# Performance work log

Measured on AMD Instinct MI355X. Metric: run time of the kernel, lower is better.

## Reference

```python
import jax, jax.numpy as jnp
import numpy as np

N, H, W, CIN, C = 2048, 19, 19, 256, 32
EPS = 1e-3

def setup_inputs() -> dict:
    key = jax.random.key(0)
    ks = jax.random.split(key, 14)
    return {
        "x": jax.random.normal(ks[0], (N, H, W, CIN), jnp.float32),
        "w_p": jax.random.normal(ks[1], (CIN, C), jnp.float32) * 0.05,
        "w_g": jax.random.normal(ks[2], (CIN, C), jnp.float32) * 0.05,
        "beta_g": jax.random.normal(ks[3], (C,), jnp.float32) * 0.1,
        "mean_g": jax.random.normal(ks[4], (C,), jnp.float32) * 0.1,
        "var_g": jax.random.uniform(ks[5], (C,), jnp.float32, 0.5, 1.5),
        "w_bias": jax.random.normal(ks[6], (2 * C, C), jnp.float32) * 0.1,
        "b_bias": jax.random.normal(ks[7], (C,), jnp.float32) * 0.1,
        "beta_p": jax.random.normal(ks[8], (C,), jnp.float32) * 0.1,
        "mean_p": jax.random.normal(ks[9], (C,), jnp.float32) * 0.1,
        "var_p": jax.random.uniform(ks[10], (C,), jnp.float32, 0.5, 1.5),
        "w_out": jax.random.normal(ks[11], (C, 2), jnp.float32) * 0.1,
        "w_pass": jax.random.normal(ks[12], (2 * C, 2), jnp.float32) * 0.1,
        "b_pass": jax.random.normal(ks[13], (2,), jnp.float32) * 0.1,
    }

def reference(x, w_p, w_g, beta_g, mean_g, var_g, w_bias, b_bias,
              beta_p, mean_p, var_p, w_out, w_pass, b_pass):
    # 1x1 convs (no bias) == channel matmuls
    p = jnp.einsum('nhwc,cd->nhwd', x, w_p)            # [N,H,W,C]
    g = jnp.einsum('nhwc,cd->nhwd', x, w_g)            # [N,H,W,C]
    # BN (scale=False, inference stats) + relu on g
    g = (g - mean_g) / jnp.sqrt(var_g + EPS) + beta_g
    g = jax.nn.relu(g)
    # global pool: per-channel mean & max over spatial dims -> [N, 2C]
    g_pooled = jnp.concatenate([g.mean(axis=(1, 2)), g.max(axis=(1, 2))], axis=1)
    # channelwise broadcast bias from pooled features
    bias = g_pooled @ w_bias + b_bias                  # [N,C]
    p = p + bias[:, None, None, :]
    # BN (scale=False) + relu on p
    p = (p - mean_p) / jnp.sqrt(var_p + EPS) + beta_p
    p = jax.nn.relu(p)
    # move logits: 1x1 conv to 2 channels
    pi = jnp.einsum('nhwc,ck->nhwk', p, w_out)         # [N,H,W,2]
    pass_logits = g_pooled @ w_pass + b_pass - 3.0     # [N,2]
    n = x.shape[0]
    pi_main = jnp.concatenate([pi[..., 0].reshape(n, -1), pass_logits[:, 0:1]], axis=1)
    pi_aux = jnp.concatenate([pi[..., 1].reshape(n, -1), pass_logits[:, 1:2]], axis=1)
    return pi_main, pi_aux
```

## Files before the change

kernel.cpp:

```cpp
#include <hip/hip_runtime.h>


#define N_IMG 2048
#define HW    361
#define CIN   256
#define C     32
#define NPIX  (N_IMG * HW)
#define EPSV  1e-3f

#define MT 256
#define KT 32
#define NT 64

#define WS_P_OFF    0
#define WS_PSUM_OFF ((size_t)NPIX * 32)
#define WS_PMAX_OFF (WS_PSUM_OFF + (size_t)N_IMG * C)
#define WS_BIAS_OFF (WS_PMAX_OFF + (size_t)N_IMG * C)

__global__ __launch_bounds__(256, 2) void k1_gemm_pool(
    const float* __restrict__ x,
    const float* __restrict__ w_p, const float* __restrict__ w_g,
    const float* __restrict__ beta_g, const float* __restrict__ mean_g,
    const float* __restrict__ var_g, float* __restrict__ ws)
{
    __shared__ float xs[KT][MT];
    __shared__ float wsh[KT][NT];

    const int t  = threadIdx.x;
    const int tm = t >> 3;
    const int tn = t & 7;
    const long P0 = (long)blockIdx.x * MT;

    float acc[8][8];
#pragma unroll
    for (int i = 0; i < 8; ++i)
#pragma unroll
        for (int j = 0; j < 8; ++j) acc[i][j] = 0.f;

    const float* xrow = x + (P0 + t) * (long)CIN;
    const int wr = t >> 3, wpart = t & 7;

    for (int k0 = 0; k0 < CIN; k0 += KT) {
#pragma unroll
        for (int i = 0; i < KT / 4; ++i) {
            float4 v = *(const float4*)(xrow + k0 + i * 4);
            xs[i * 4 + 0][t] = v.x;
            xs[i * 4 + 1][t] = v.y;
            xs[i * 4 + 2][t] = v.z;
            xs[i * 4 + 3][t] = v.w;
        }
        {
            const float* src = (wpart < 4) ? (w_p + (long)(k0 + wr) * C + wpart * 8)
                                           : (w_g + (long)(k0 + wr) * C + (wpart - 4) * 8);
            float4 v0 = *(const float4*)(src);
            float4 v1 = *(const float4*)(src + 4);
            *(float4*)(&wsh[wr][wpart * 8])     = v0;
            *(float4*)(&wsh[wr][wpart * 8 + 4]) = v1;
        }
        __syncthreads();
#pragma unroll
        for (int kk = 0; kk < KT; ++kk) {
            float a[8], b[8];
            *(float4*)(a)     = *(const float4*)(&xs[kk][tm * 8]);
            *(float4*)(a + 4) = *(const float4*)(&xs[kk][tm * 8 + 4]);
            *(float4*)(b)     = *(const float4*)(&wsh[kk][tn * 8]);
            *(float4*)(b + 4) = *(const float4*)(&wsh[kk][tn * 8 + 4]);
#pragma unroll
            for (int i = 0; i < 8; ++i)
#pragma unroll
                for (int j = 0; j < 8; ++j)
                    acc[i][j] = fmaf(a[i], b[j], acc[i][j]);
        }
        __syncthreads();
    }

    if (tn < 4) {
        float* wp_out = ws + WS_P_OFF;
#pragma unroll
        for (int i = 0; i < 8; ++i) {
            long pix = P0 + tm * 8 + i;
            float4 v0 = make_float4(acc[i][0], acc[i][1], acc[i][2], acc[i][3]);
            float4 v1 = make_float4(acc[i][4], acc[i][5], acc[i][6], acc[i][7]);
            *(float4*)(wp_out + pix * 32 + tn * 8)     = v0;
            *(float4*)(wp_out + pix * 32 + tn * 8 + 4) = v1;
        }
    }

    float gsum[2][8], gmax[2][8];
#pragma unroll
    for (int s = 0; s < 2; ++s)
#pragma unroll
        for (int j = 0; j < 8; ++j) { gsum[s][j] = 0.f; gmax[s][j] = 0.f; }

    const int  n0 = (int)(P0 / HW);
    const long Bnd = (long)(n0 + 1) * HW;

    if (tn >= 4) {
#pragma unroll
        for (int j = 0; j < 8; ++j) {
            int c = (tn - 4) * 8 + j;
            float rs = rsqrtf(var_g[c] + EPSV);
            float mg = mean_g[c], bg = beta_g[c];
#pragma unroll
            for (int i = 0; i < 8; ++i) {
                long pix = P0 + tm * 8 + i;
                float g = fmaxf((acc[i][j] - mg) * rs + bg, 0.f);
                int s = (pix >= Bnd) ? 1 : 0;
                gsum[s][j] += g;
                gmax[s][j] = fmaxf(gmax[s][j], g);
            }
        }
    }

#pragma unroll
    for (int s = 0; s < 2; ++s)
#pragma unroll
        for (int j = 0; j < 8; ++j) {
            float v = gsum[s][j], m = gmax[s][j];
            v += __shfl_xor(v, 8, 64);  m = fmaxf(m, __shfl_xor(m, 8, 64));
            v += __shfl_xor(v, 16, 64); m = fmaxf(m, __shfl_xor(m, 16, 64));
            v += __shfl_xor(v, 32, 64); m = fmaxf(m, __shfl_xor(m, 32, 64));
            gsum[s][j] = v; gmax[s][j] = m;
        }

    const int lane = t & 63;
    if (tn >= 4 && (lane >> 3) == 0) {
        float* psum = ws + WS_PSUM_OFF;
        int*   pmax = (int*)(ws + WS_PMAX_OFF);
#pragma unroll
        for (int s = 0; s < 2; ++s) {
            int n = n0 + s;
            bool active = (s == 0) || (Bnd < P0 + MT && n < N_IMG);
            if (active) {
#pragma unroll
                for (int j = 0; j < 8; ++j) {
                    int c = (tn - 4) * 8 + j;
                    atomicAdd(psum + n * C + c, gsum[s][j]);
                    atomicMax(pmax + n * C + c, __float_as_int(gmax[s][j]));
                }
            }
        }
    }
}

__global__ void k2_bias(const float* __restrict__ psum,
                        const float* __restrict__ pmax,
                        const float* __restrict__ w_bias,
                        const float* __restrict__ b_bias,
                        const float* __restrict__ w_pass,
                        const float* __restrict__ b_pass,
                        float* __restrict__ ws_bias,
                        float* __restrict__ out)
{
    const int n = blockIdx.x;
    const int t = threadIdx.x;
    __shared__ float gp[64];
    if (t < 32) gp[t] = psum[n * 32 + t] * (1.f / (float)HW);
    else        gp[t] = pmax[n * 32 + (t - 32)];
    __syncthreads();
    if (t < 32) {
        float acc = b_bias[t];
#pragma unroll
        for (int j = 0; j < 64; ++j) acc = fmaf(gp[j], w_bias[j * 32 + t], acc);
        ws_bias[n * 32 + t] = acc;
    } else if (t < 34) {
        int k = t - 32;
        float acc = b_pass[k] - 3.0f;
#pragma unroll
        for (int j = 0; j < 64; ++j) acc = fmaf(gp[j], w_pass[j * 2 + k], acc);
        out[(size_t)k * ((size_t)N_IMG * 362) + (size_t)n * 362 + 361] = acc;
    }
}

__global__ __launch_bounds__(256) void k3_epilogue(
    const float* __restrict__ ws_p, const float* __restrict__ ws_bias,
    const float* __restrict__ beta_p, const float* __restrict__ mean_p,
    const float* __restrict__ var_p, const float* __restrict__ w_out,
    float* __restrict__ out)
{
    const long pix = (long)blockIdx.x * 256 + threadIdx.x;
    const int n  = (int)(pix / HW);
    const int hw = (int)(pix - (long)n * HW);

    float p[32], b[32];
    const float4* pr = (const float4*)(ws_p + pix * 32);
    const float4* br = (const float4*)(ws_bias + (long)n * 32);
#pragma unroll
    for (int i = 0; i < 8; ++i) ((float4*)p)[i] = pr[i];
#pragma unroll
    for (int i = 0; i < 8; ++i) ((float4*)b)[i] = br[i];

    float a0 = 0.f, a1 = 0.f;
#pragma unroll
    for (int c = 0; c < 32; ++c) {
        float v = (p[c] + b[c] - mean_p[c]) * rsqrtf(var_p[c] + EPSV) + beta_p[c];
        v = fmaxf(v, 0.f);
        a0 = fmaf(v, w_out[c * 2 + 0], a0);
        a1 = fmaf(v, w_out[c * 2 + 1], a1);
    }
    out[(size_t)n * 362 + hw] = a0;
    out[(size_t)N_IMG * 362 + (size_t)n * 362 + hw] = a1;
}

extern "C" void kernel_launch(void* const* d_in, const int* in_sizes, int n_in,
                              void* d_out, int out_size, void* d_ws, size_t ws_size,
                              hipStream_t stream)
{
    const float* x      = (const float*)d_in[0];
    const float* w_p    = (const float*)d_in[1];
    const float* w_g    = (const float*)d_in[2];
    const float* beta_g = (const float*)d_in[3];
    const float* mean_g = (const float*)d_in[4];
    const float* var_g  = (const float*)d_in[5];
    const float* w_bias = (const float*)d_in[6];
    const float* b_bias = (const float*)d_in[7];
    const float* beta_p = (const float*)d_in[8];
    const float* mean_p = (const float*)d_in[9];
    const float* var_p  = (const float*)d_in[10];
    const float* w_out  = (const float*)d_in[11];
    const float* w_pass = (const float*)d_in[12];
    const float* b_pass = (const float*)d_in[13];
    float* out = (float*)d_out;
    float* ws  = (float*)d_ws;
    (void)in_sizes; (void)n_in; (void)out_size; (void)ws_size;

    hipMemsetAsync(ws + WS_PSUM_OFF, 0, 2u * N_IMG * C * sizeof(float), stream);

    k1_gemm_pool<<<NPIX / MT, 256, 0, stream>>>(x, w_p, w_g, beta_g, mean_g, var_g, ws);
    k2_bias<<<N_IMG, 64, 0, stream>>>(ws + WS_PSUM_OFF, ws + WS_PMAX_OFF,
                                      w_bias, b_bias, w_pass, b_pass,
                                      ws + WS_BIAS_OFF, out);
    k3_epilogue<<<NPIX / 256, 256, 0, stream>>>(ws + WS_P_OFF, ws + WS_BIAS_OFF,
                                                beta_p, mean_p, var_p, w_out, out);
}
```

Measured before the change: 1.116 ms.

## Use split-bf16 MFMA for the 1x1 conv GEMM and fuse bias into epilogue

Replaces the FP32 FMA GEMM with bf16 MFMA instructions, using a hi/lo split of both operands (three MFMAs per tile) to approximate FP32 accuracy. Weights are pre-split and transposed into workspace by a new prep kernel and staged whole in shared memory. The separate bias and epilogue kernels are merged into one per-image kernel that folds the BN and bias into a per-channel scale and offset. The split-bf16 scheme gives slightly lower accuracy than full FP32, and x is now read straight from global memory into registers without shared-memory staging.

```diff
diff --git a/kernel.cpp b/kernel.cpp
--- a/kernel.cpp
+++ b/kernel.cpp
@@ -1,4 +1,5 @@
 #include <hip/hip_runtime.h>
+#include <hip/hip_bf16.h>
 
 
 #define N_IMG 2048
@@ -7,199 +8,225 @@
 #define C     32
 #define NPIX  (N_IMG * HW)
 #define EPSV  1e-3f
-
-#define MT 256
-#define KT 32
-#define NT 64
+#define OUT_HALF (N_IMG * 362)
+
+#define KPAD  264
 
 #define WS_P_OFF    0
 #define WS_PSUM_OFF ((size_t)NPIX * 32)
 #define WS_PMAX_OFF (WS_PSUM_OFF + (size_t)N_IMG * C)
-#define WS_BIAS_OFF (WS_PMAX_OFF + (size_t)N_IMG * C)
+#define WS_WT_OFF   (WS_PMAX_OFF + (size_t)N_IMG * C)
+
+typedef __attribute__((ext_vector_type(8))) short short8;
+typedef __attribute__((ext_vector_type(4))) float f32x4;
+
+static __device__ __forceinline__ short f2bf(float f) {
+    __hip_bfloat16 h = __float2bfloat16(f);
+    return *reinterpret_cast<short*>(&h);
+}
+static __device__ __forceinline__ float bf2f(short s) {
+    unsigned int u = ((unsigned int)(unsigned short)s) << 16;
+    return __builtin_bit_cast(float, u);
+}
+
+__global__ void k0_prep(const float* __restrict__ w_p, const float* __restrict__ w_g,
+                        unsigned short* __restrict__ wt)
+{
+    const int col = blockIdx.x;
+    const int t = threadIdx.x;
+#pragma unroll
+    for (int it = 0; it < 2; ++it) {
+        int kk = t + it * 256;
+        if (kk < KPAD) {
+            unsigned short hi = 0, lo = 0;
+            if (kk < CIN) {
+                float f = (col < C) ? w_p[kk * C + col] : w_g[kk * C + (col - C)];
+                short h = f2bf(f);
+                hi = (unsigned short)h;
+                lo = (unsigned short)f2bf(f - bf2f(h));
+            }
+            wt[col * KPAD + kk] = hi;
+            wt[64 * KPAD + col * KPAD + kk] = lo;
+        }
+    }
+}
 
 __global__ __launch_bounds__(256, 2) void k1_gemm_pool(
     const float* __restrict__ x,
-    const float* __restrict__ w_p, const float* __restrict__ w_g,
+    const unsigned short* __restrict__ wt_g,
     const float* __restrict__ beta_g, const float* __restrict__ mean_g,
-    const float* __restrict__ var_g, float* __restrict__ ws)
-{
-    __shared__ float xs[KT][MT];
-    __shared__ float wsh[KT][NT];
-
-    const int t  = threadIdx.x;
-    const int tm = t >> 3;
-    const int tn = t & 7;
-    const long P0 = (long)blockIdx.x * MT;
-
-    float acc[8][8];
-#pragma unroll
-    for (int i = 0; i < 8; ++i)
-#pragma unroll
-        for (int j = 0; j < 8; ++j) acc[i][j] = 0.f;
-
-    const float* xrow = x + (P0 + t) * (long)CIN;
-    const int wr = t >> 3, wpart = t & 7;
-
-    for (int k0 = 0; k0 < CIN; k0 += KT) {
-#pragma unroll
-        for (int i = 0; i < KT / 4; ++i) {
-            float4 v = *(const float4*)(xrow + k0 + i * 4);
-            xs[i * 4 + 0][t] = v.x;
-            xs[i * 4 + 1][t] = v.y;
-            xs[i * 4 + 2][t] = v.z;
-            xs[i * 4 + 3][t] = v.w;
-        }
-        {
-            const float* src = (wpart < 4) ? (w_p + (long)(k0 + wr) * C + wpart * 8)
-                                           : (w_g + (long)(k0 + wr) * C + (wpart - 4) * 8);
-            float4 v0 = *(const float4*)(src);
-            float4 v1 = *(const float4*)(src + 4);
-            *(float4*)(&wsh[wr][wpart * 8])     = v0;
-            *(float4*)(&wsh[wr][wpart * 8 + 4]) = v1;
-        }
-        __syncthreads();
-#pragma unroll
-        for (int kk = 0; kk < KT; ++kk) {
-            float a[8], b[8];
-            *(float4*)(a)     = *(const float4*)(&xs[kk][tm * 8]);
-            *(float4*)(a + 4) = *(const float4*)(&xs[kk][tm * 8 + 4]);
-            *(float4*)(b)     = *(const float4*)(&wsh[kk][tn * 8]);
-            *(float4*)(b + 4) = *(const float4*)(&wsh[kk][tn * 8 + 4]);
-#pragma unroll
-            for (int i = 0; i < 8; ++i)
-#pragma unroll
-                for (int j = 0; j < 8; ++j)
-                    acc[i][j] = fmaf(a[i], b[j], acc[i][j]);
-        }
-        __syncthreads();
-    }
-
-    if (tn < 4) {
-        float* wp_out = ws + WS_P_OFF;
-#pragma unroll
-        for (int i = 0; i < 8; ++i) {
-            long pix = P0 + tm * 8 + i;
-            float4 v0 = make_float4(acc[i][0], acc[i][1], acc[i][2], acc[i][3]);
-            float4 v1 = make_float4(acc[i][4], acc[i][5], acc[i][6], acc[i][7]);
-            *(float4*)(wp_out + pix * 32 + tn * 8)     = v0;
-            *(float4*)(wp_out + pix * 32 + tn * 8 + 4) = v1;
-        }
-    }
-
-    float gsum[2][8], gmax[2][8];
-#pragma unroll
-    for (int s = 0; s < 2; ++s)
-#pragma unroll
-        for (int j = 0; j < 8; ++j) { gsum[s][j] = 0.f; gmax[s][j] = 0.f; }
-
-    const int  n0 = (int)(P0 / HW);
-    const long Bnd = (long)(n0 + 1) * HW;
-
-    if (tn >= 4) {
-#pragma unroll
-        for (int j = 0; j < 8; ++j) {
-            int c = (tn - 4) * 8 + j;
-            float rs = rsqrtf(var_g[c] + EPSV);
-            float mg = mean_g[c], bg = beta_g[c];
-#pragma unroll
-            for (int i = 0; i < 8; ++i) {
-                long pix = P0 + tm * 8 + i;
-                float g = fmaxf((acc[i][j] - mg) * rs + bg, 0.f);
-                int s = (pix >= Bnd) ? 1 : 0;
-                gsum[s][j] += g;
-                gmax[s][j] = fmaxf(gmax[s][j], g);
-            }
-        }
-    }
-
-#pragma unroll
-    for (int s = 0; s < 2; ++s)
-#pragma unroll
-        for (int j = 0; j < 8; ++j) {
-            float v = gsum[s][j], m = gmax[s][j];
-            v += __shfl_xor(v, 8, 64);  m = fmaxf(m, __shfl_xor(m, 8, 64));
-            v += __shfl_xor(v, 16, 64); m = fmaxf(m, __shfl_xor(m, 16, 64));
-            v += __shfl_xor(v, 32, 64); m = fmaxf(m, __shfl_xor(m, 32, 64));
-            gsum[s][j] = v; gmax[s][j] = m;
-        }
-
-    const int lane = t & 63;
-    if (tn >= 4 && (lane >> 3) == 0) {
-        float* psum = ws + WS_PSUM_OFF;
-        int*   pmax = (int*)(ws + WS_PMAX_OFF);
-#pragma unroll
-        for (int s = 0; s < 2; ++s) {
-            int n = n0 + s;
-            bool active = (s == 0) || (Bnd < P0 + MT && n < N_IMG);
-            if (active) {
-#pragma unroll
-                for (int j = 0; j < 8; ++j) {
-                    int c = (tn - 4) * 8 + j;
-                    atomicAdd(psum + n * C + c, gsum[s][j]);
-                    atomicMax(pmax + n * C + c, __float_as_int(gmax[s][j]));
-                }
-            }
-        }
-    }
-}
-
-__global__ void k2_bias(const float* __restrict__ psum,
-                        const float* __restrict__ pmax,
-                        const float* __restrict__ w_bias,
-                        const float* __restrict__ b_bias,
-                        const float* __restrict__ w_pass,
-                        const float* __restrict__ b_pass,
-                        float* __restrict__ ws_bias,
-                        float* __restrict__ out)
+    const float* __restrict__ var_g,
+    float* __restrict__ ws_p, float* __restrict__ psum, int* __restrict__ pmax)
+{
+    __shared__ uint4 smem4[2 * 64 * KPAD * 2 / 16];
+    const unsigned short* wt_hi_l = (const unsigned short*)smem4;
+    const unsigned short* wt_lo_l = wt_hi_l + 64 * KPAD;
+
+    const int t = threadIdx.x;
+    {
+        const uint4* src = (const uint4*)wt_g;
+        for (int i = t; i < 4224; i += 256) smem4[i] = src[i];
+    }
+    __syncthreads();
+
+    const int wave = t >> 6, lane = t & 63;
+    const int lr = lane & 15, lk = lane >> 4;
+    const int W0 = blockIdx.x * 256 + wave * 64;
+
+    f32x4 acc[4][4];
+#pragma unroll
+    for (int m = 0; m < 4; ++m)
+#pragma unroll
+        for (int n = 0; n < 4; ++n) acc[m][n] = (f32x4){0.f, 0.f, 0.f, 0.f};
+
+    const float* ap = x + (size_t)(W0 + lr) * CIN + lk * 8;
+
+    for (int k0 = 0; k0 < CIN; k0 += 32) {
+        float4 av[4][2];
+#pragma unroll
+        for (int m = 0; m < 4; ++m) {
+            const float* p = ap + (size_t)m * 16 * CIN + k0;
+            av[m][0] = *(const float4*)p;
+            av[m][1] = *(const float4*)(p + 4);
+        }
+        short8 bh[4], bl[4];
+#pragma unroll
+        for (int n = 0; n < 4; ++n) {
+            int idx = (n * 16 + lr) * KPAD + k0 + lk * 8;
+            bh[n] = *(const short8*)(wt_hi_l + idx);
+            bl[n] = *(const short8*)(wt_lo_l + idx);
+        }
+        short8 ah[4], al[4];
+#pragma unroll
+        for (int m = 0; m < 4; ++m) {
+            float fa[8];
+            *(float4*)(fa) = av[m][0]; *(float4*)(fa + 4) = av[m][1];
+#pragma unroll
+            for (int j = 0; j < 8; ++j) {
+                short h = f2bf(fa[j]);
+                ah[m][j] = h;
+                al[m][j] = f2bf(fa[j] - bf2f(h));
+            }
+        }
+#pragma unroll
+        for (int m = 0; m < 4; ++m)
+#pragma unroll
+            for (int n = 0; n < 4; ++n) {
+                acc[m][n] = __builtin_amdgcn_mfma_f32_16x16x32_bf16(ah[m], bh[n], acc[m][n], 0, 0, 0);
+                acc[m][n] = __builtin_amdgcn_mfma_f32_16x16x32_bf16(al[m], bh[n], acc[m][n], 0, 0, 0);
+                acc[m][n] = __builtin_amdgcn_mfma_f32_16x16x32_bf16(ah[m], bl[n], acc[m][n], 0, 0, 0);
+            }
+    }
+
+#pragma unroll
+    for (int m = 0; m < 4; ++m)
+#pragma unroll
+        for (int n = 0; n < 2; ++n)
+#pragma unroll
+            for (int r = 0; r < 4; ++r) {
+                int pix = W0 + m * 16 + lk * 4 + r;
+                ws_p[(size_t)pix * 32 + n * 16 + lr] = acc[m][n][r];
+            }
+
+    const int n0w = W0 / HW;
+    const int Bnd = (n0w + 1) * HW;
+    float gs0[2] = {0.f, 0.f}, gs1[2] = {0.f, 0.f};
+    float gm0[2] = {0.f, 0.f}, gm1[2] = {0.f, 0.f};
+#pragma unroll
+    for (int n = 0; n < 2; ++n) {
+        const int cg = n * 16 + lr;
+        const float rs = rsqrtf(var_g[cg] + EPSV);
+        const float mg = mean_g[cg], bg = beta_g[cg];
+#pragma unroll
+        for (int m = 0; m < 4; ++m)
+#pragma unroll
+            for (int r = 0; r < 4; ++r) {
+                int pix = W0 + m * 16 + lk * 4 + r;
+                float g = fmaxf((acc[m][n + 2][r] - mg) * rs + bg, 0.f);
+                bool s1 = (pix >= Bnd);
+                gs0[n] += s1 ? 0.f : g;
+                gs1[n] += s1 ? g : 0.f;
+                gm0[n] = fmaxf(gm0[n], s1 ? 0.f : g);
+                gm1[n] = fmaxf(gm1[n], s1 ? g : 0.f);
+            }
+    }
+#pragma unroll
+    for (int n = 0; n < 2; ++n) {
+        gs0[n] += __shfl_xor(gs0[n], 16, 64); gs0[n] += __shfl_xor(gs0[n], 32, 64);
+        gs1[n] += __shfl_xor(gs1[n], 16, 64); gs1[n] += __shfl_xor(gs1[n], 32, 64);
+        gm0[n] = fmaxf(gm0[n], __shfl_xor(gm0[n], 16, 64));
+        gm0[n] = fmaxf(gm0[n], __shfl_xor(gm0[n], 32, 64));
+        gm1[n] = fmaxf(gm1[n], __shfl_xor(gm1[n], 16, 64));
+        gm1[n] = fmaxf(gm1[n], __shfl_xor(gm1[n], 32, 64));
+    }
+    if (lk == 0) {
+#pragma unroll
+        for (int n = 0; n < 2; ++n) {
+            int c = n * 16 + lr;
+            atomicAdd(psum + n0w * C + c, gs0[n]);
+            atomicMax(pmax + n0w * C + c, __float_as_int(gm0[n]));
+        }
+        if (Bnd < W0 + 64) {
+#pragma unroll
+            for (int n = 0; n < 2; ++n) {
+                int c = n * 16 + lr;
+                atomicAdd(psum + (n0w + 1) * C + c, gs1[n]);
+                atomicMax(pmax + (n0w + 1) * C + c, __float_as_int(gm1[n]));
+            }
+        }
+    }
+}
+
+__global__ __launch_bounds__(256) void k2_epilogue(
+    const float* __restrict__ psum, const int* __restrict__ pmax,
+    const float* __restrict__ w_bias, const float* __restrict__ b_bias,
+    const float* __restrict__ w_pass, const float* __restrict__ b_pass,
+    const float* __restrict__ beta_p, const float* __restrict__ mean_p,
+    const float* __restrict__ var_p, const float* __restrict__ w_out,
+    const float* __restrict__ ws_p, float* __restrict__ out)
 {
     const int n = blockIdx.x;
     const int t = threadIdx.x;
     __shared__ float gp[64];
-    if (t < 32) gp[t] = psum[n * 32 + t] * (1.f / (float)HW);
-    else        gp[t] = pmax[n * 32 + (t - 32)];
+    __shared__ float rs_s[32], off_s[32], wo0_s[32], wo1_s[32];
+
+    if (t < 32)      gp[t] = psum[n * 32 + t] * (1.0f / (float)HW);
+    else if (t < 64) gp[t] = __int_as_float(pmax[n * 32 + (t - 32)]);
     __syncthreads();
+
     if (t < 32) {
-        float acc = b_bias[t];
-#pragma unroll
-        for (int j = 0; j < 64; ++j) acc = fmaf(gp[j], w_bias[j * 32 + t], acc);
-        ws_bias[n * 32 + t] = acc;
+        float bias = b_bias[t];
+#pragma unroll
+        for (int j = 0; j < 64; ++j) bias = fmaf(gp[j], w_bias[j * 32 + t], bias);
+        float rs = rsqrtf(var_p[t] + EPSV);
+        rs_s[t] = rs;
+        off_s[t] = (bias - mean_p[t]) * rs + beta_p[t];
+        wo0_s[t] = w_out[t * 2 + 0];
+        wo1_s[t] = w_out[t * 2 + 1];
     } else if (t < 34) {
         int k = t - 32;
-        float acc = b_pass[k] - 3.0f;
-#pragma unroll
-        for (int j = 0; j < 64; ++j) acc = fmaf(gp[j], w_pass[j * 2 + k], acc);
-        out[(size_t)k * ((size_t)N_IMG * 362) + (size_t)n * 362 + 361] = acc;
-    }
-}
-
-__global__ __launch_bounds__(256) void k3_epilogue(
-    const float* __restrict__ ws_p, const float* __restrict__ ws_bias,
-    const float* __restrict__ beta_p, const float* __restrict__ mean_p,
-    const float* __restrict__ var_p, const float* __restrict__ w_out,
-    float* __restrict__ out)
-{
-    const long pix = (long)blockIdx.x * 256 + threadIdx.x;
-    const int n  = (int)(pix / HW);
-    const int hw = (int)(pix - (long)n * HW);
-
-    float p[32], b[32];
-    const float4* pr = (const float4*)(ws_p + pix * 32);
-    const float4* br = (const float4*)(ws_bias + (long)n * 32);
-#pragma unroll
-    for (int i = 0; i < 8; ++i) ((float4*)p)[i] = pr[i];
-#pragma unroll
-    for (int i = 0; i < 8; ++i) ((float4*)b)[i] = br[i];
-
-    float a0 = 0.f, a1 = 0.f;
-#pragma unroll
-    for (int c = 0; c < 32; ++c) {
-        float v = (p[c] + b[c] - mean_p[c]) * rsqrtf(var_p[c] + EPSV) + beta_p[c];
-        v = fmaxf(v, 0.f);
-        a0 = fmaf(v, w_out[c * 2 + 0], a0);
-        a1 = fmaf(v, w_out[c * 2 + 1], a1);
-    }
-    out[(size_t)n * 362 + hw] = a0;
-    out[(size_t)N_IMG * 362 + (size_t)n * 362 + hw] = a1;
+        float a = b_pass[k] - 3.0f;
+#pragma unroll
+        for (int j = 0; j < 64; ++j) a = fmaf(gp[j], w_pass[j * 2 + k], a);
+        out[(size_t)k * OUT_HALF + (size_t)n * 362 + 361] = a;
+    }
+    __syncthreads();
+
+    for (int i = t; i < HW; i += 256) {
+        const float* pr = ws_p + ((size_t)n * HW + i) * 32;
+        float p[32];
+#pragma unroll
+        for (int q = 0; q < 8; ++q) ((float4*)p)[q] = ((const float4*)pr)[q];
+        float a0 = 0.f, a1 = 0.f;
+#pragma unroll
+        for (int c = 0; c < 32; ++c) {
+            float v = fmaxf(fmaf(p[c], rs_s[c], off_s[c]), 0.f);
+            a0 = fmaf(v, wo0_s[c], a0);
+            a1 = fmaf(v, wo1_s[c], a1);
+        }
+        out[(size_t)n * 362 + i] = a0;
+        out[(size_t)OUT_HALF + (size_t)n * 362 + i] = a1;
+    }
 }
 
 extern "C" void kernel_launch(void* const* d_in, const int* in_sizes, int n_in,
@@ -226,10 +253,12 @@
 
     hipMemsetAsync(ws + WS_PSUM_OFF, 0, 2u * N_IMG * C * sizeof(float), stream);
 
-    k1_gemm_pool<<<NPIX / MT, 256, 0, stream>>>(x, w_p, w_g, beta_g, mean_g, var_g, ws);
-    k2_bias<<<N_IMG, 64, 0, stream>>>(ws + WS_PSUM_OFF, ws + WS_PMAX_OFF,
-                                      w_bias, b_bias, w_pass, b_pass,
-                                      ws + WS_BIAS_OFF, out);
-    k3_epilogue<<<NPIX / 256, 256, 0, stream>>>(ws + WS_P_OFF, ws + WS_BIAS_OFF,
-                                                beta_p, mean_p, var_p, w_out, out);
-}
+    k0_prep<<<64, 256, 0, stream>>>(w_p, w_g, (unsigned short*)(ws + WS_WT_OFF));
+    k1_gemm_pool<<<NPIX / 256, 256, 0, stream>>>(
+        x, (const unsigned short*)(ws + WS_WT_OFF), beta_g, mean_g, var_g,
+        ws + WS_P_OFF, ws + WS_PSUM_OFF, (int*)(ws + WS_PMAX_OFF));
+    k2_epilogue<<<N_IMG, 256, 0, stream>>>(
+        ws + WS_PSUM_OFF, (const int*)(ws + WS_PMAX_OFF),
+        w_bias, b_bias, w_pass, b_pass, beta_p, mean_p, var_p, w_out,
+        ws + WS_P_OFF, out);
+}
```

Measured after the change: 1.041 ms. 6.8% less time.
